# Optimization experiments

Hardware: AMD Instinct MI355X
Metric: run time of the kernel (lower is better)

The kernel has to match this reference:

```python
import jax, jax.numpy as jnp
import numpy as np

MODEL_DIM = 256
PAIR_IMPORTANCE_WEIGHT = 0.5
B, S, D = 4, 4096, MODEL_DIM


def setup_inputs() -> dict:
    key = jax.random.key(0)
    ks = jax.random.split(key, 6)
    return {
        "query": jax.random.normal(ks[0], (B, S, D), dtype=jnp.float32),
        "key": jax.random.normal(ks[1], (B, S, D), dtype=jnp.float32),
        "value": jax.random.normal(ks[2], (B, S, D), dtype=jnp.float32),
        "W_query": jax.random.normal(ks[3], (D, D), dtype=jnp.float32),
        "W_key": jax.random.normal(ks[4], (D, D), dtype=jnp.float32),
        "W_value": jax.random.normal(ks[5], (D, D), dtype=jnp.float32),
    }


def reference(query, key, value, W_query, W_key, W_value):
    # Projections: [B,S,D] @ [D,D]
    q = jnp.einsum('bsd,de->bse', query, W_query)
    k = jnp.einsum('bsd,de->bse', key, W_key)
    v = jnp.einsum('bsd,de->bse', value, W_value)
    scale = jnp.sqrt(jnp.asarray(MODEL_DIM, dtype=q.dtype))
    # Full [B,S,S] score matrix (global max forces materialization)
    scores = jnp.einsum('bqd,bkd->bqk', q, k) / scale
    s_len = scores.shape[1]
    diag_bias = jnp.eye(s_len, dtype=scores.dtype) * jnp.max(scores)
    scores = scores + PAIR_IMPORTANCE_WEIGHT * diag_bias  # broadcast over batch
    attention_weights = jax.nn.softmax(scores, axis=-1)
    output = jnp.einsum('bqk,bkd->bqd', attention_weights, v)
    return output, attention_weights
```

## Files before the change

### kernel.cpp

```cpp
#include <hip/hip_runtime.h>
#include <cstdint>
#include <cstddef>

#define BB 4
#define SS 4096
#define DD 256
#define SCORE_SCALE (1.0f/16.0f)
#define PIW 0.5f
#define NROWS (BB * SS)

typedef float          f32x4  __attribute__((ext_vector_type(4)));
typedef __bf16         bf16v8 __attribute__((ext_vector_type(8)));
typedef unsigned short u16v8  __attribute__((ext_vector_type(8)));
typedef unsigned short u16v4  __attribute__((ext_vector_type(4)));

__device__ __forceinline__ f32x4 mfma_bf16(u16v8 a, u16v8 b, f32x4 c) {
    return __builtin_amdgcn_mfma_f32_16x16x32_bf16(
        __builtin_bit_cast(bf16v8, a), __builtin_bit_cast(bf16v8, b), c, 0, 0, 0);
}

__device__ __forceinline__ unsigned short f2bf(float f) {
    unsigned u = __float_as_uint(f);
    u += 0x7FFFu + ((u >> 16) & 1u);
    return (unsigned short)(u >> 16);
}
__device__ __forceinline__ float bf2f(unsigned short h) {
    return __uint_as_float(((unsigned)h) << 16);
}
__device__ __forceinline__ unsigned fenc(float x) {
    unsigned u = __float_as_uint(x);
    return (u & 0x80000000u) ? ~u : (u | 0x80000000u);
}
__device__ __forceinline__ float fdec(unsigned e) {
    return __uint_as_float((e & 0x80000000u) ? (e ^ 0x80000000u) : ~e);
}

#define PSPAD 42

__global__ __launch_bounds__(256) void proj_kernel(
    const float* __restrict__ query, const float* __restrict__ key_, const float* __restrict__ value,
    const float* __restrict__ Wq, const float* __restrict__ Wk, const float* __restrict__ Wv,
    unsigned short* __restrict__ qh, unsigned short* __restrict__ ql,
    unsigned short* __restrict__ kh, unsigned short* __restrict__ kl,
    unsigned short* __restrict__ vT, unsigned* __restrict__ gmax)
{
    const int z = blockIdx.z;
    const float* A = (z == 0) ? query : (z == 1) ? key_ : value;
    const float* W = (z == 0) ? Wq    : (z == 1) ? Wk   : Wv;
    if (z == 0 && blockIdx.x == 0 && blockIdx.y == 0 && threadIdx.x == 0)
        *gmax = 0x007FFFFFu;

    __shared__ unsigned short Ah[128][PSPAD];
    __shared__ unsigned short Al[128][PSPAD];
    __shared__ unsigned short Bh[128][PSPAD];
    __shared__ unsigned short Bl[128][PSPAD];

    const int tid = threadIdx.x;
    const int lane = tid & 63, w = tid >> 6;
    const int wr = (w >> 1) * 64, wc = (w & 1) * 64;
    const int m = lane & 15, qq = lane >> 4;
    const int rowBase = blockIdx.y * 128;
    const int colBase = blockIdx.x * 128;

    f32x4 acc[4][4];
    #pragma unroll
    for (int i = 0; i < 4; i++)
        #pragma unroll
        for (int j = 0; j < 4; j++)
            acc[i][j] = (f32x4){0.f, 0.f, 0.f, 0.f};

    const int chunk = (tid & 3) * 8;
    const int srow  = tid >> 2;

    for (int k0 = 0; k0 < DD; k0 += 32) {
        #pragma unroll
        for (int i = 0; i < 2; i++) {
            int r = srow + i * 64;
            const float* src = &A[(size_t)(rowBase + r) * DD + k0 + chunk];
            float4 f0 = *(const float4*)src;
            float4 f1 = *(const float4*)(src + 4);
            float v[8] = {f0.x, f0.y, f0.z, f0.w, f1.x, f1.y, f1.z, f1.w};
            u16v8 h, l;
            #pragma unroll
            for (int e = 0; e < 8; e++) {
                h[e] = f2bf(v[e]);
                l[e] = f2bf(v[e] - bf2f(h[e]));
            }
            *(u16v8*)&Ah[r][chunk] = h;
            *(u16v8*)&Al[r][chunk] = l;
        }
        #pragma unroll
        for (int i = 0; i < 4; i++) {
            int idx = tid + i * 256;
            int kk = idx >> 5, nq = idx & 31;
            float4 f = *(const float4*)&W[(size_t)(k0 + kk) * DD + colBase + nq * 4];
            float v[4] = {f.x, f.y, f.z, f.w};
            #pragma unroll
            for (int e = 0; e < 4; e++) {
                unsigned short h = f2bf(v[e]);
                unsigned short l = f2bf(v[e] - bf2f(h));
                Bh[nq * 4 + e][kk] = h;
                Bl[nq * 4 + e][kk] = l;
            }
        }
        __syncthreads();

        const int kb = qq * 8;
        u16v8 ah[4], al[4], bh[4], bl[4];
        #pragma unroll
        for (int i = 0; i < 4; i++) {
            ah[i] = *(const u16v8*)&Ah[wr + i * 16 + m][kb];
            al[i] = *(const u16v8*)&Al[wr + i * 16 + m][kb];
            bh[i] = *(const u16v8*)&Bh[wc + i * 16 + m][kb];
            bl[i] = *(const u16v8*)&Bl[wc + i * 16 + m][kb];
        }
        #pragma unroll
        for (int i = 0; i < 4; i++)
            #pragma unroll
            for (int j = 0; j < 4; j++) {
                acc[i][j] = mfma_bf16(ah[i], bh[j], acc[i][j]);
                acc[i][j] = mfma_bf16(ah[i], bl[j], acc[i][j]);
                acc[i][j] = mfma_bf16(al[i], bh[j], acc[i][j]);
            }
        __syncthreads();
    }

    #pragma unroll
    for (int i = 0; i < 4; i++) {
        #pragma unroll
        for (int j = 0; j < 4; j++) {
            #pragma unroll
            for (int r = 0; r < 4; r++) {
                const int gr  = rowBase + wr + i * 16 + qq * 4 + r;
                const int col = colBase + wc + j * 16 + m;
                const float v = acc[i][j][r];
                if (z == 2) {
                    const int b2 = gr >> 12, s2 = gr & (SS - 1);
                    size_t idx = ((((size_t)b2 * 16 + (col >> 4)) * 128 + (s2 >> 5)) * 64
                                  + ((col & 15) | (((s2 >> 3) & 3) << 4))) * 8 + (s2 & 7);
                    vT[idx] = f2bf(v);
                } else {
                    unsigned short h = f2bf(v);
                    unsigned short l = f2bf(v - bf2f(h));
                    unsigned short* H = (z == 0) ? qh : kh;
                    unsigned short* L = (z == 0) ? ql : kl;
                    H[(size_t)gr * DD + col] = h;
                    L[(size_t)gr * DD + col] = l;
                }
            }
        }
    }
}

#define SPAD 40

__global__ __launch_bounds__(256) void scores_mfma(
    const unsigned short* __restrict__ qh, const unsigned short* __restrict__ ql,
    const unsigned short* __restrict__ kh, const unsigned short* __restrict__ kl,
    float* __restrict__ attn, unsigned* __restrict__ gmax,
    float* __restrict__ tmaxg, float* __restrict__ tsumg)
{
    const int b = blockIdx.z;
    const size_t boff = (size_t)b * SS * DD;
    const unsigned short* Qh = qh + boff;
    const unsigned short* Ql = ql + boff;
    const unsigned short* Kh = kh + boff;
    const unsigned short* Kl = kl + boff;
    float* C = attn + (size_t)b * SS * SS;

    __shared__ unsigned short Ah[128][SPAD];
    __shared__ unsigned short Al[128][SPAD];
    __shared__ unsigned short Bh[128][SPAD];
    __shared__ unsigned short Bl[128][SPAD];
    __shared__ float s_m[4][64];
    __shared__ float s_s[4][64];
    __shared__ float red[128];

    const int tid = threadIdx.x;
    const int lane = tid & 63, w = tid >> 6;
    const int wr = (w >> 1) * 64, wc = (w & 1) * 64;
    const int m = lane & 15, qq = lane >> 4;
    const int rowBase = blockIdx.y * 128;
    const int colBase = blockIdx.x * 128;

    f32x4 acc[4][4];
    #pragma unroll
    for (int i = 0; i < 4; i++)
        #pragma unroll
        for (int j = 0; j < 4; j++)
            acc[i][j] = (f32x4){0.f, 0.f, 0.f, 0.f};

    const int chunk = (tid & 3) * 8;
    const int srow  = tid >> 2;

    for (int k0 = 0; k0 < DD; k0 += 32) {
        #pragma unroll
        for (int i = 0; i < 2; i++) {
            int r = srow + i * 64;
            size_t ga = (size_t)(rowBase + r) * DD + k0 + chunk;
            size_t gb = (size_t)(colBase + r) * DD + k0 + chunk;
            *(u16v8*)&Ah[r][chunk] = *(const u16v8*)&Qh[ga];
            *(u16v8*)&Al[r][chunk] = *(const u16v8*)&Ql[ga];
            *(u16v8*)&Bh[r][chunk] = *(const u16v8*)&Kh[gb];
            *(u16v8*)&Bl[r][chunk] = *(const u16v8*)&Kl[gb];
        }
        __syncthreads();

        const int kb = qq * 8;
        u16v8 ah[4], al[4], bh[4], bl[4];
        #pragma unroll
        for (int i = 0; i < 4; i++) {
            ah[i] = *(const u16v8*)&Ah[wr + i * 16 + m][kb];
            al[i] = *(const u16v8*)&Al[wr + i * 16 + m][kb];
            bh[i] = *(const u16v8*)&Bh[wc + i * 16 + m][kb];
            bl[i] = *(const u16v8*)&Bl[wc + i * 16 + m][kb];
        }
        #pragma unroll
        for (int i = 0; i < 4; i++)
            #pragma unroll
            for (int j = 0; j < 4; j++) {
                acc[i][j] = mfma_bf16(ah[i], bh[j], acc[i][j]);
                acc[i][j] = mfma_bf16(ah[i], bl[j], acc[i][j]);
                acc[i][j] = mfma_bf16(al[i], bh[j], acc[i][j]);
            }
        __syncthreads();
    }

    #pragma unroll
    for (int i = 0; i < 4; i++)
        #pragma unroll
        for (int j = 0; j < 4; j++)
            acc[i][j] *= SCORE_SCALE;

    float lmax[16];
    #pragma unroll
    for (int i = 0; i < 4; i++)
        #pragma unroll
        for (int r = 0; r < 4; r++)
            lmax[i * 4 + r] = fmaxf(fmaxf(acc[i][0][r], acc[i][1][r]),
                                    fmaxf(acc[i][2][r], acc[i][3][r]));
    #pragma unroll
    for (int t = 0; t < 16; t++) {
        #pragma unroll
        for (int msk = 1; msk < 16; msk <<= 1)
            lmax[t] = fmaxf(lmax[t], __shfl_xor(lmax[t], msk));
    }
    if (m == 0) {
        #pragma unroll
        for (int i = 0; i < 4; i++)
            #pragma unroll
            for (int r = 0; r < 4; r++)
                s_m[w][i * 16 + qq * 4 + r] = lmax[i * 4 + r];
    }
    __syncthreads();
    float lsum[16];
    #pragma unroll
    for (int i = 0; i < 4; i++)
        #pragma unroll
        for (int r = 0; r < 4; r++) {
            int idx = i * 16 + qq * 4 + r;
            float rm = fmaxf(s_m[w][idx], s_m[w ^ 1][idx]);
            float s = 0.f;
            #pragma unroll
            for (int j = 0; j < 4; j++)
                s += __expf(acc[i][j][r] - rm);
            lsum[i * 4 + r] = s;
        }
    #pragma unroll
    for (int t = 0; t < 16; t++) {
        #pragma unroll
        for (int msk = 1; msk < 16; msk <<= 1)
            lsum[t] += __shfl_xor(lsum[t], msk);
    }
    if (m == 0) {
        #pragma unroll
        for (int i = 0; i < 4; i++)
            #pragma unroll
            for (int r = 0; r < 4; r++)
                s_s[w][i * 16 + qq * 4 + r] = lsum[i * 4 + r];
    }
    __syncthreads();

    if (tid < 128) {
        int wp = tid >> 6, lr = tid & 63;
        float tm = fmaxf(s_m[2 * wp][lr], s_m[2 * wp + 1][lr]);
        float ts = s_s[2 * wp][lr] + s_s[2 * wp + 1][lr];
        size_t gi = (size_t)blockIdx.x * NROWS + (size_t)b * SS + rowBase + tid;
        tmaxg[gi] = tm;
        tsumg[gi] = ts;
        red[tid] = tm;
    }
    __syncthreads();
    for (int s2 = 64; s2 > 0; s2 >>= 1) {
        if (tid < s2) red[tid] = fmaxf(red[tid], red[tid + s2]);
        __syncthreads();
    }
    if (tid == 0) atomicMax(gmax, fenc(red[0]));

    #pragma unroll
    for (int i = 0; i < 4; i++)
        #pragma unroll
        for (int j = 0; j < 4; j++)
            #pragma unroll
            for (int r = 0; r < 4; r++) {
                int row = rowBase + wr + i * 16 + qq * 4 + r;
                int col = colBase + wc + j * 16 + m;
                __builtin_nontemporal_store(acc[i][j][r], &C[(size_t)row * SS + col]);
            }
}

__global__ __launch_bounds__(256) void stats_merge(
    const float* __restrict__ tmaxg, const float* __restrict__ tsumg,
    const float* __restrict__ attn, const unsigned* __restrict__ gmax,
    float* __restrict__ rowm, float* __restrict__ rowinv)
{
    const int grow = blockIdx.x * 256 + threadIdx.x;
    const int b = grow >> 12, i = grow & (SS - 1);
    const float bias = PIW * fdec(*gmax);

    float tm[32];
    float mx = -INFINITY;
    #pragma unroll
    for (int t = 0; t < 32; t++) {
        tm[t] = tmaxg[(size_t)t * NROWS + grow];
        mx = fmaxf(mx, tm[t]);
    }
    const float dii = attn[(size_t)b * SS * SS + (size_t)i * SS + i];
    mx = fmaxf(mx, dii + bias);

    float s = 0.f;
    #pragma unroll
    for (int t = 0; t < 32; t++)
        s += tsumg[(size_t)t * NROWS + grow] * __expf(tm[t] - mx);
    s += __expf(dii + bias - mx) - __expf(dii - mx);

    rowm[grow] = mx;
    rowinv[grow] = 1.0f / s;
}

#define AVBK 256

__global__ __launch_bounds__(256) void av_softmax_mfma(
    float* __restrict__ attn, const unsigned short* __restrict__ vT,
    const float* __restrict__ rowm, const float* __restrict__ rowinv,
    const unsigned* __restrict__ gmax, float* __restrict__ out)
{
    const int lin = blockIdx.x;
    const int b = (lin & 7) >> 1;
    const int rowTile = ((lin >> 3) << 1) | (lin & 1);
    const int rowBase = rowTile * 32;

    float* A = attn + (size_t)b * SS * SS;
    const unsigned short* Bf = vT + (size_t)b * (16 * 128 * 64 * 8);
    const float bias = PIW * fdec(*gmax);

    __shared__ unsigned short As[2][32][264];

    const int tid = threadIdx.x;
    const int lane = tid & 63, w = tid >> 6;
    const int m = lane & 15, qq = lane >> 4;

    const int ra = tid >> 3;
    const int c8 = tid & 7;
    const int rr = rowBase + ra;
    float* Arow = A + (size_t)rr * SS;
    const float mr = rowm[b * SS + rr];
    const float ri = rowinv[b * SS + rr];

    f32x4 acc[2][4];
    #pragma unroll
    for (int i = 0; i < 2; i++)
        #pragma unroll
        for (int j = 0; j < 4; j++)
            acc[i][j] = (f32x4){0.f, 0.f, 0.f, 0.f};

    f32x4 pf[8];

    auto loadA = [&](int kbase) {
        #pragma unroll
        for (int u = 0; u < 8; u++)
            pf[u] = *(const f32x4*)&Arow[kbase + c8 * 4 + u * 32];
    };
    auto procStore = [&](int kbase, int buf) {
        #pragma unroll
        for (int u = 0; u < 8; u++) {
            int c = c8 * 4 + u * 32;
            int j0 = kbase + c;
            float e0 = pf[u][0] + ((j0 + 0 == rr) ? bias : 0.0f);
            float e1 = pf[u][1] + ((j0 + 1 == rr) ? bias : 0.0f);
            float e2 = pf[u][2] + ((j0 + 2 == rr) ? bias : 0.0f);
            float e3 = pf[u][3] + ((j0 + 3 == rr) ? bias : 0.0f);
            float w0 = __expf(e0 - mr) * ri;
            float w1 = __expf(e1 - mr) * ri;
            float w2 = __expf(e2 - mr) * ri;
            float w3 = __expf(e3 - mr) * ri;
            f32x4 wv = (f32x4){w0, w1, w2, w3};
            __builtin_nontemporal_store(wv, (f32x4*)&Arow[j0]);
            *(u16v4*)&As[buf][ra][c] =
                (u16v4){f2bf(w0), f2bf(w1), f2bf(w2), f2bf(w3)};
        }
    };

    const int NT = SS / AVBK;

    loadA(0);
    procStore(0, 0);
    __syncthreads();

    for (int t = 0; t < NT; t++) {
        const int k0 = t * AVBK;
        const int cur = t & 1;
        if (t + 1 < NT)
            loadA(k0 + AVBK);
        #pragma unroll
        for (int kk = 0; kk < 8; kk++) {
            const int kb = kk * 32 + qq * 8;
            const int kkg = (k0 >> 5) + kk;
            u16v8 bf_[4], af_[2];
            #pragma unroll
            for (int j = 0; j < 4; j++)
                bf_[j] = *(const u16v8*)&Bf[(((size_t)(w * 4 + j) * 128 + kkg) * 64 + lane) * 8];
            #pragma unroll
            for (int i = 0; i < 2; i++)
                af_[i] = *(const u16v8*)&As[cur][i * 16 + m][kb];
            #pragma unroll
            for (int i = 0; i < 2; i++)
                #pragma unroll
                for (int j = 0; j < 4; j++)
                    acc[i][j] = mfma_bf16(af_[i], bf_[j], acc[i][j]);
        }
        if (t + 1 < NT) {
            procStore(k0 + AVBK, cur ^ 1);
            __syncthreads();
        }
    }

    #pragma unroll
    for (int i = 0; i < 2; i++) {
        #pragma unroll
        for (int j = 0; j < 4; j++) {
            #pragma unroll
            for (int r = 0; r < 4; r++) {
                int row = rowBase + i * 16 + qq * 4 + r;
                int col = w * 64 + j * 16 + m;
                __builtin_nontemporal_store(
                    acc[i][j][r], &out[((size_t)b * SS + row) * DD + col]);
            }
        }
    }
}

extern "C" void kernel_launch(void* const* d_in, const int* in_sizes, int n_in,
                              void* d_out, int out_size, void* d_ws, size_t ws_size,
                              hipStream_t stream)
{
    const float* query = (const float*)d_in[0];
    const float* key_  = (const float*)d_in[1];
    const float* value = (const float*)d_in[2];
    const float* Wq    = (const float*)d_in[3];
    const float* Wk    = (const float*)d_in[4];
    const float* Wv    = (const float*)d_in[5];

    float* out  = (float*)d_out;
    float* attn = out + (size_t)BB * SS * DD;

    const size_t E = (size_t)BB * SS * DD;
    unsigned short* qh = (unsigned short*)d_ws;
    unsigned short* ql = qh + E;
    unsigned short* kh = ql + E;
    unsigned short* kl = kh + E;
    unsigned short* vT = kl + E;
    float* tmaxg  = (float*)(vT + E);
    float* tsumg  = tmaxg + 32 * (size_t)NROWS;
    float* rowm   = tsumg + 32 * (size_t)NROWS;
    float* rowinv = rowm + NROWS;
    unsigned* gmax = (unsigned*)(rowinv + NROWS);

    proj_kernel<<<dim3(DD / 128, (BB * SS) / 128, 3), 256, 0, stream>>>(
        query, key_, value, Wq, Wk, Wv, qh, ql, kh, kl, vT, gmax);
    scores_mfma<<<dim3(SS / 128, SS / 128, BB), 256, 0, stream>>>(
        qh, ql, kh, kl, attn, gmax, tmaxg, tsumg);
    stats_merge<<<dim3(NROWS / 256), 256, 0, stream>>>(
        tmaxg, tsumg, attn, gmax, rowm, rowinv);
    av_softmax_mfma<<<dim3(512), 256, 0, stream>>>(
        attn, vT, rowm, rowinv, gmax, out);
}
```

Measured before the change: 631.3 us.

## Store Q/K in MFMA fragment layout and load scores operands directly from global

The projection kernel now writes the hi/lo bf16 Q and K halves in a pre-swizzled MFMA fragment order, matching how vT was already stored. The scores kernel drops its LDS staging and per-k-step barriers and loads each 16-row fragment straight from global memory as one contiguous 16-byte load per lane. The grid becomes 1D with a block-index remap that spreads batches and tiles across dispatch order, presumably for cache locality. The cost is that the LDS reuse across waves goes away, so each wave fetches its own operand fragments and relies on L2 and L1 for sharing.

```diff
diff --git a/kernel.cpp b/kernel.cpp
--- a/kernel.cpp
+++ b/kernel.cpp
@@ -33,6 +33,11 @@
 }
 __device__ __forceinline__ float fdec(unsigned e) {
     return __uint_as_float((e & 0x80000000u) ? (e ^ 0x80000000u) : ~e);
+}
+
+__device__ __forceinline__ size_t fragidx(int growFlat, int k, int kPerRow32) {
+    return ((((size_t)(growFlat >> 4) * kPerRow32 + (k >> 5)) * 64)
+            + ((growFlat & 15) | (((k >> 3) & 3) << 4))) * 8 + (k & 7);
 }
 
 #define PSPAD 42
@@ -136,23 +141,22 @@
                 const float v = acc[i][j][r];
                 if (z == 2) {
                     const int b2 = gr >> 12, s2 = gr & (SS - 1);
-                    size_t idx = ((((size_t)b2 * 16 + (col >> 4)) * 128 + (s2 >> 5)) * 64
-                                  + ((col & 15) | (((s2 >> 3) & 3) << 4))) * 8 + (s2 & 7);
+                    size_t idx = (size_t)b2 * (16 * 128 * 512)
+                               + fragidx(col, s2, 128);
                     vT[idx] = f2bf(v);
                 } else {
                     unsigned short h = f2bf(v);
                     unsigned short l = f2bf(v - bf2f(h));
                     unsigned short* H = (z == 0) ? qh : kh;
                     unsigned short* L = (z == 0) ? ql : kl;
-                    H[(size_t)gr * DD + col] = h;
-                    L[(size_t)gr * DD + col] = l;
+                    size_t idx = fragidx(gr, col, 8);
+                    H[idx] = h;
+                    L[idx] = l;
                 }
             }
         }
     }
 }
-
-#define SPAD 40
 
 __global__ __launch_bounds__(256) void scores_mfma(
     const unsigned short* __restrict__ qh, const unsigned short* __restrict__ ql,
@@ -160,18 +164,15 @@
     float* __restrict__ attn, unsigned* __restrict__ gmax,
     float* __restrict__ tmaxg, float* __restrict__ tsumg)
 {
-    const int b = blockIdx.z;
-    const size_t boff = (size_t)b * SS * DD;
-    const unsigned short* Qh = qh + boff;
-    const unsigned short* Ql = ql + boff;
-    const unsigned short* Kh = kh + boff;
-    const unsigned short* Kl = kl + boff;
+    const int lin = blockIdx.x;
+    const int b = (lin & 7) >> 1;
+    const int t2 = ((lin >> 3) << 1) | (lin & 1);
+    const int bx = t2 & 31, by = t2 >> 5;
+    const int rowBase = by * 128;
+    const int colBase = bx * 128;
+
     float* C = attn + (size_t)b * SS * SS;
 
-    __shared__ unsigned short Ah[128][SPAD];
-    __shared__ unsigned short Al[128][SPAD];
-    __shared__ unsigned short Bh[128][SPAD];
-    __shared__ unsigned short Bl[128][SPAD];
     __shared__ float s_m[4][64];
     __shared__ float s_s[4][64];
     __shared__ float red[128];
@@ -180,8 +181,6 @@
     const int lane = tid & 63, w = tid >> 6;
     const int wr = (w >> 1) * 64, wc = (w & 1) * 64;
     const int m = lane & 15, qq = lane >> 4;
-    const int rowBase = blockIdx.y * 128;
-    const int colBase = blockIdx.x * 128;
 
     f32x4 acc[4][4];
     #pragma unroll
@@ -190,30 +189,20 @@
         for (int j = 0; j < 4; j++)
             acc[i][j] = (f32x4){0.f, 0.f, 0.f, 0.f};
 
-    const int chunk = (tid & 3) * 8;
-    const int srow  = tid >> 2;
-
-    for (int k0 = 0; k0 < DD; k0 += 32) {
-        #pragma unroll
-        for (int i = 0; i < 2; i++) {
-            int r = srow + i * 64;
-            size_t ga = (size_t)(rowBase + r) * DD + k0 + chunk;
-            size_t gb = (size_t)(colBase + r) * DD + k0 + chunk;
-            *(u16v8*)&Ah[r][chunk] = *(const u16v8*)&Qh[ga];
-            *(u16v8*)&Al[r][chunk] = *(const u16v8*)&Ql[ga];
-            *(u16v8*)&Bh[r][chunk] = *(const u16v8*)&Kh[gb];
-            *(u16v8*)&Bl[r][chunk] = *(const u16v8*)&Kl[gb];
-        }
-        __syncthreads();
-
-        const int kb = qq * 8;
+    const size_t ta = ((size_t)b * SS + rowBase + wr) >> 4;
+    const size_t tb = ((size_t)b * SS + colBase + wc) >> 4;
+
+    #pragma unroll 2
+    for (int kk = 0; kk < 8; kk++) {
         u16v8 ah[4], al[4], bh[4], bl[4];
         #pragma unroll
         for (int i = 0; i < 4; i++) {
-            ah[i] = *(const u16v8*)&Ah[wr + i * 16 + m][kb];
-            al[i] = *(const u16v8*)&Al[wr + i * 16 + m][kb];
-            bh[i] = *(const u16v8*)&Bh[wc + i * 16 + m][kb];
-            bl[i] = *(const u16v8*)&Bl[wc + i * 16 + m][kb];
+            const size_t fa = (((ta + i) * 8 + kk) * 64 + lane) * 8;
+            const size_t fb = (((tb + i) * 8 + kk) * 64 + lane) * 8;
+            ah[i] = *(const u16v8*)&qh[fa];
+            al[i] = *(const u16v8*)&ql[fa];
+            bh[i] = *(const u16v8*)&kh[fb];
+            bl[i] = *(const u16v8*)&kl[fb];
         }
         #pragma unroll
         for (int i = 0; i < 4; i++)
@@ -223,7 +212,6 @@
                 acc[i][j] = mfma_bf16(ah[i], bl[j], acc[i][j]);
                 acc[i][j] = mfma_bf16(al[i], bh[j], acc[i][j]);
             }
-        __syncthreads();
     }
 
     #pragma unroll
@@ -285,7 +273,7 @@
         int wp = tid >> 6, lr = tid & 63;
         float tm = fmaxf(s_m[2 * wp][lr], s_m[2 * wp + 1][lr]);
         float ts = s_s[2 * wp][lr] + s_s[2 * wp + 1][lr];
-        size_t gi = (size_t)blockIdx.x * NROWS + (size_t)b * SS + rowBase + tid;
+        size_t gi = (size_t)bx * NROWS + (size_t)b * SS + rowBase + tid;
         tmaxg[gi] = tm;
         tsumg[gi] = ts;
         red[tid] = tm;
@@ -351,7 +339,7 @@
     const int rowBase = rowTile * 32;
 
     float* A = attn + (size_t)b * SS * SS;
-    const unsigned short* Bf = vT + (size_t)b * (16 * 128 * 64 * 8);
+    const unsigned short* Bf = vT + (size_t)b * (16 * 128 * 512);
     const float bias = PIW * fdec(*gmax);
 
     __shared__ unsigned short As[2][32][264];
@@ -478,7 +466,7 @@
 
     proj_kernel<<<dim3(DD / 128, (BB * SS) / 128, 3), 256, 0, stream>>>(
         query, key_, value, Wq, Wk, Wv, qh, ql, kh, kl, vT, gmax);
-    scores_mfma<<<dim3(SS / 128, SS / 128, BB), 256, 0, stream>>>(
+    scores_mfma<<<dim3(4096), 256, 0, stream>>>(
         qh, ql, kh, kl, attn, gmax, tmaxg, tsumg);
     stats_merge<<<dim3(NROWS / 256), 256, 0, stream>>>(
         tmaxg, tsumg, attn, gmax, rowm, rowinv);
```

Measured after the change: 615.4 us. -2.5%, faster.
